# Optimization experiments

Measured on AMD Instinct MI355X. Metric: run time of the kernel, lower is better.

## Reference

```python
import jax, jax.numpy as jnp
import numpy as np

B, C, W, H = 4, 256, 64, 64
AC = C // 4  # attn channels


def setup_inputs() -> dict:
    key = jax.random.key(0)
    ks = jax.random.split(key, 4)
    x = jax.random.normal(ks[0], (B, C, W, H), dtype=jnp.float32)
    Wq = jax.random.normal(ks[1], (AC, C), dtype=jnp.float32) * (1.0 / np.sqrt(C))
    Wk = jax.random.normal(ks[2], (AC, C), dtype=jnp.float32) * (1.0 / np.sqrt(C))
    Wv = jax.random.normal(ks[3], (C, C), dtype=jnp.float32) * (1.0 / np.sqrt(C))
    bq = jnp.zeros((AC,), dtype=jnp.float32)
    bk = jnp.zeros((AC,), dtype=jnp.float32)
    bv = jnp.zeros((C,), dtype=jnp.float32)
    gamma = jnp.zeros((1,), dtype=jnp.float32)
    return {"x": x, "Wq": Wq, "bq": bq, "Wk": Wk, "bk": bk, "Wv": Wv, "bv": bv, "gamma": gamma}


def reference(x, Wq, bq, Wk, bk, Wv, bv, gamma):
    b, c, w, h = x.shape
    n = w * h
    xf = x.reshape(b, c, n)  # [B, C, N]
    # 1x1 convs == channel GEMMs
    q = jnp.einsum('oc,bcn->bon', Wq, xf) + bq[None, :, None]  # [B, AC, N]
    k = jnp.einsum('oc,bcn->bon', Wk, xf) + bk[None, :, None]  # [B, AC, N]
    v = jnp.einsum('oc,bcn->bon', Wv, xf) + bv[None, :, None]  # [B, C, N]
    # attn[b, i, j] = sum_c q[b, c, i] * k[b, c, j]  (query transposed)
    attn = jnp.einsum('bci,bcj->bij', q, k)  # [B, N, N]
    # NOTE: non-standard softmax over dim=1 (over query index i for each column j)
    attn = jax.nn.softmax(attn, axis=1)
    # attn_out = attn @ value.T  -> [B, N, C]
    attn_out = jnp.einsum('bij,bcj->bic', attn, v)
    attn_out = attn_out.reshape(b, w, h, c).transpose(0, 3, 1, 2)  # [B, C, W, H]
    return gamma[0] * attn_out + x
```

## Files before the change

### kernel.cpp

```cpp
#include <hip/hip_runtime.h>
#include <hip/hip_bf16.h>

#define BB 4
#define CC 256
#define NN 4096
#define AC2 64
#define PP 76

typedef __attribute__((ext_vector_type(4))) float f32x4;
typedef __attribute__((ext_vector_type(8))) short bf16x8;

__device__ __forceinline__ short f2bf(float f) {
    unsigned u = __builtin_bit_cast(unsigned, f);
    u = u + 0x7FFFu + ((u >> 16) & 1u);
    return (short)(u >> 16);
}

__global__ __launch_bounds__(256) void prep_kernel(
    const float* __restrict__ Wq, const float* __restrict__ Wk,
    const float* __restrict__ Wv, short* __restrict__ Wb)
{
    const int idx = (blockIdx.x * 256 + threadIdx.x) * 4;
    const int o = idx >> 8, c = idx & 255;
    const float* row = (o < 64) ? (Wq + o * CC)
                     : (o < 128) ? (Wk + (o - 64) * CC)
                                 : (Wv + (o - 128) * CC);
    float4 v = *(const float4*)&row[c];
    short4 s4;
    s4.x = f2bf(v.x); s4.y = f2bf(v.y); s4.z = f2bf(v.z); s4.w = f2bf(v.w);
    *(short4*)&Wb[idx] = s4;
}

__global__ __launch_bounds__(512) void qkv_kernel(
    const float* __restrict__ x, const short* __restrict__ Wb,
    const float* __restrict__ bq, const float* __restrict__ bk,
    const float* __restrict__ bv,
    short* __restrict__ Qt, short* __restrict__ Kt, short* __restrict__ V)
{
    __shared__ __align__(16) short Xl[32 * 72];
    const int bid0 = blockIdx.x;
    const int bid = ((bid0 & 7) << 6) | (bid0 >> 3);
    const int b = bid >> 7;
    const int n0 = (bid & 127) << 5;
    const int tid = threadIdx.x;
    const int lane = tid & 63, w = tid >> 6;
    const int l15 = lane & 15, lh = lane >> 4;

    f32x4 acc[3][2];
#pragma unroll
    for (int i = 0; i < 3; ++i)
#pragma unroll
        for (int j = 0; j < 2; ++j) acc[i][j] = (f32x4){0.f, 0.f, 0.f, 0.f};

    for (int ck = 0; ck < 4; ++ck) {
        const int c0 = ck << 6;
        bf16x8 Af[3][2];
#pragma unroll
        for (int of = 0; of < 3; ++of)
#pragma unroll
            for (int ks = 0; ks < 2; ++ks)
                Af[of][ks] = *(const bf16x8*)&Wb[(size_t)(w * 48 + of * 16 + l15) * CC +
                                                 c0 + ks * 32 + (lh << 3)];
        {
            const int cr = tid >> 3, q4 = tid & 7;
            float4 v = *(const float4*)&x[((size_t)(b * CC + c0 + cr)) * NN + n0 + q4 * 4];
            Xl[(q4 * 4 + 0) * 72 + cr] = f2bf(v.x);
            Xl[(q4 * 4 + 1) * 72 + cr] = f2bf(v.y);
            Xl[(q4 * 4 + 2) * 72 + cr] = f2bf(v.z);
            Xl[(q4 * 4 + 3) * 72 + cr] = f2bf(v.w);
        }
        __syncthreads();
#pragma unroll
        for (int ks = 0; ks < 2; ++ks) {
            const int co = ks * 32 + (lh << 3);
            bf16x8 Bf[2];
#pragma unroll
            for (int nf = 0; nf < 2; ++nf)
                Bf[nf] = *(const bf16x8*)&Xl[(nf * 16 + l15) * 72 + co];
#pragma unroll
            for (int of = 0; of < 3; ++of)
#pragma unroll
                for (int nf = 0; nf < 2; ++nf)
                    acc[of][nf] = __builtin_amdgcn_mfma_f32_16x16x32_bf16(
                        Af[of][ks], Bf[nf], acc[of][nf], 0, 0, 0);
        }
        __syncthreads();
    }
#pragma unroll
    for (int of = 0; of < 3; ++of) {
        const int obase = w * 48 + of * 16 + (lh << 2);
        float bias[4];
#pragma unroll
        for (int r = 0; r < 4; ++r) {
            int o = obase + r;
            bias[r] = (o < 64) ? bq[o] : (o < 128) ? bk[o - 64] : bv[o - 128];
        }
#pragma unroll
        for (int nf = 0; nf < 2; ++nf) {
            const int n = n0 + nf * 16 + l15;
            if (obase < 128) {
                short4 pk;
                pk.x = f2bf(acc[of][nf][0] + bias[0]);
                pk.y = f2bf(acc[of][nf][1] + bias[1]);
                pk.z = f2bf(acc[of][nf][2] + bias[2]);
                pk.w = f2bf(acc[of][nf][3] + bias[3]);
                short* dst = (obase < 64)
                    ? (Qt + ((size_t)b * NN + n) * AC2 + obase)
                    : (Kt + ((size_t)b * NN + n) * AC2 + (obase - 64));
                *(short4*)dst = pk;
            } else {
#pragma unroll
                for (int r = 0; r < 4; ++r) {
                    int o = obase + r - 128;
                    V[(((size_t)b * CC + o) * NN) + n] = f2bf(acc[of][nf][r] + bias[r]);
                }
            }
        }
    }
}

__global__ __launch_bounds__(256) void stats_kernel(
    const short* __restrict__ Qt, const short* __restrict__ Kt,
    float* __restrict__ tArr)
{
    const int bid0 = blockIdx.x;
    const int bid = ((bid0 & 7) << 7) | (bid0 >> 3);
    const int b = bid >> 8;
    const int j0 = (bid & 255) << 4;
    const int tid = threadIdx.x;
    const int lane = tid & 63, w = tid >> 6;
    const int l15 = lane & 15, lh = lane >> 4;
    const short* Qb = Qt + (size_t)b * NN * AC2;

    bf16x8 Bf[2];
#pragma unroll
    for (int ks = 0; ks < 2; ++ks)
        Bf[ks] = *(const bf16x8*)&Kt[((size_t)b * NN + j0 + l15) * AC2 +
                                     ks * 32 + (lh << 3)];

    bf16x8 A0[4], A1[4];
#pragma unroll
    for (int f = 0; f < 4; ++f) {
        const size_t rowA = (size_t)(w * 1024 + f * 16 + l15);
        A0[f] = *(const bf16x8*)&Qb[rowA * AC2 + (lh << 3)];
        A1[f] = *(const bf16x8*)&Qb[rowA * AC2 + 32 + (lh << 3)];
    }

    float m_run = -INFINITY, l_run = 0.f;
    for (int ii = 0; ii < 16; ++ii) {
        bf16x8 A0n[4], A1n[4];
        const int in0 = w * 1024 + ((ii + 1) & 15) * 64;
#pragma unroll
        for (int f = 0; f < 4; ++f) {
            const size_t rowA = (size_t)(in0 + f * 16 + l15);
            A0n[f] = *(const bf16x8*)&Qb[rowA * AC2 + (lh << 3)];
            A1n[f] = *(const bf16x8*)&Qb[rowA * AC2 + 32 + (lh << 3)];
        }
        f32x4 s[4];
#pragma unroll
        for (int f = 0; f < 4; ++f) {
            f32x4 t = (f32x4){0.f, 0.f, 0.f, 0.f};
            t = __builtin_amdgcn_mfma_f32_16x16x32_bf16(A0[f], Bf[0], t, 0, 0, 0);
            t = __builtin_amdgcn_mfma_f32_16x16x32_bf16(A1[f], Bf[1], t, 0, 0, 0);
            s[f] = t;
        }
        float mx = s[0][0];
#pragma unroll
        for (int f = 0; f < 4; ++f)
#pragma unroll
            for (int r = 0; r < 4; ++r) mx = fmaxf(mx, s[f][r]);
        const float m_new = fmaxf(m_run, mx);
        float add = 0.f;
#pragma unroll
        for (int f = 0; f < 4; ++f)
#pragma unroll
            for (int r = 0; r < 4; ++r) add += __expf(s[f][r] - m_new);
        l_run = l_run * __expf(m_run - m_new) + add;
        m_run = m_new;
#pragma unroll
        for (int f = 0; f < 4; ++f) { A0[f] = A0n[f]; A1[f] = A1n[f]; }
    }
#pragma unroll
    for (int off = 16; off <= 32; off <<= 1) {
        float m2 = __shfl_xor(m_run, off);
        float l2 = __shfl_xor(l_run, off);
        float mm = fmaxf(m_run, m2);
        l_run = l_run * __expf(m_run - mm) + l2 * __expf(m2 - mm);
        m_run = mm;
    }
    __shared__ float sm[4][16];
    __shared__ float sl[4][16];
    if (lane < 16) { sm[w][lane] = m_run; sl[w][lane] = l_run; }
    __syncthreads();
    if (tid < 16) {
        float m = sm[0][tid], l = sl[0][tid];
#pragma unroll
        for (int q = 1; q < 4; ++q) {
            float m2 = sm[q][tid], l2 = sl[q][tid];
            float mm = fmaxf(m, m2);
            l = l * __expf(m - mm) + l2 * __expf(m2 - mm);
            m = mm;
        }
        tArr[(size_t)b * NN + j0 + tid] = m + __logf(l);
    }
}

__global__ __launch_bounds__(256) void out_kernel(
    const short* __restrict__ Qt, const short* __restrict__ Kt,
    const short* __restrict__ V,
    const float* __restrict__ tArr,
    const float* __restrict__ x, const float* __restrict__ gamma,
    float* __restrict__ out)
{
    __shared__ __align__(16) short Pl[2][64 * PP];
    const int bid0 = blockIdx.x;
    const int bid = ((bid0 & 7) << 6) | (bid0 >> 3);
    const int cs = bid & 1;
    const int itile = (bid >> 1) & 63;
    const int b = bid >> 7;
    const int i0 = itile << 6, c0 = cs << 7;
    const int tid = threadIdx.x;
    const int lane = tid & 63, w = tid >> 6;
    const int l15 = lane & 15, lh = lane >> 4;
    const int iw = i0 + (w << 4);

    const short* Ktb = Kt + (size_t)b * NN * AC2;
    const float* tb  = tArr + (size_t)b * NN;
    const short* Vb  = V + ((size_t)b * CC + c0 + (w << 5)) * NN;

    bf16x8 Aq[2];
#pragma unroll
    for (int ks = 0; ks < 2; ++ks)
        Aq[ks] = *(const bf16x8*)&Qt[((size_t)b * NN + iw + l15) * AC2 +
                                     ks * 32 + (lh << 3)];

    f32x4 acc[4][2];
#pragma unroll
    for (int f = 0; f < 4; ++f)
#pragma unroll
        for (int cf = 0; cf < 2; ++cf) acc[f][cf] = (f32x4){0.f, 0.f, 0.f, 0.f};

    bf16x8 Kc[4][2], Vc[2][2];
    float tc[4];
#pragma unroll
    for (int jf = 0; jf < 4; ++jf) {
#pragma unroll
        for (int ks = 0; ks < 2; ++ks)
            Kc[jf][ks] = *(const bf16x8*)&Ktb[(size_t)(jf * 16 + l15) * AC2 +
                                              ks * 32 + (lh << 3)];
        tc[jf] = tb[jf * 16 + l15];
    }
#pragma unroll
    for (int cf = 0; cf < 2; ++cf)
#pragma unroll
        for (int ks = 0; ks < 2; ++ks)
            Vc[cf][ks] = *(const bf16x8*)&Vb[(size_t)(cf * 16 + l15) * NN +
                                             ks * 32 + (lh << 3)];

    for (int jt = 0; jt < 64; ++jt) {
        const int jn = ((jt + 1) & 63) << 6;
        bf16x8 Kn[4][2], Vn[2][2];
        float tn[4];
#pragma unroll
        for (int jf = 0; jf < 4; ++jf) {
#pragma unroll
            for (int ks = 0; ks < 2; ++ks)
                Kn[jf][ks] = *(const bf16x8*)&Ktb[(size_t)(jn + jf * 16 + l15) * AC2 +
                                                  ks * 32 + (lh << 3)];
            tn[jf] = tb[jn + jf * 16 + l15];
        }
#pragma unroll
        for (int cf = 0; cf < 2; ++cf)
#pragma unroll
            for (int ks = 0; ks < 2; ++ks)
                Vn[cf][ks] = *(const bf16x8*)&Vb[(size_t)(cf * 16 + l15) * NN + jn +
                                                 ks * 32 + (lh << 3)];

        short* Plw = &Pl[jt & 1][0];
#pragma unroll
        for (int jf = 0; jf < 4; ++jf) {
            f32x4 s = (f32x4){0.f, 0.f, 0.f, 0.f};
            s = __builtin_amdgcn_mfma_f32_16x16x32_bf16(Aq[0], Kc[jf][0], s, 0, 0, 0);
            s = __builtin_amdgcn_mfma_f32_16x16x32_bf16(Aq[1], Kc[jf][1], s, 0, 0, 0);
#pragma unroll
            for (int r = 0; r < 4; ++r)
                Plw[(w * 16 + lh * 4 + r) * PP + jf * 16 + l15] =
                    f2bf(__expf(s[r] - tc[jf]));
        }
        asm volatile("s_waitcnt lgkmcnt(0)" ::: "memory");
        __builtin_amdgcn_s_barrier();
        asm volatile("" ::: "memory");
#pragma unroll
        for (int ks = 0; ks < 2; ++ks) {
#pragma unroll
            for (int f = 0; f < 4; ++f) {
                bf16x8 Ap = *(const bf16x8*)&Plw[(f * 16 + l15) * PP +
                                                 ks * 32 + (lh << 3)];
#pragma unroll
                for (int cf = 0; cf < 2; ++cf)
                    acc[f][cf] = __builtin_amdgcn_mfma_f32_16x16x32_bf16(
                        Ap, Vc[cf][ks], acc[f][cf], 0, 0, 0);
            }
        }
#pragma unroll
        for (int jf = 0; jf < 4; ++jf) {
            Kc[jf][0] = Kn[jf][0]; Kc[jf][1] = Kn[jf][1]; tc[jf] = tn[jf];
        }
#pragma unroll
        for (int cf = 0; cf < 2; ++cf) { Vc[cf][0] = Vn[cf][0]; Vc[cf][1] = Vn[cf][1]; }
    }

    __syncthreads();
    const float g = gamma[0];
    float* Pfw = (float*)&Pl[0][0] + w * 1056;
#pragma unroll
    for (int pass = 0; pass < 2; ++pass) {
#pragma unroll
        for (int fh = 0; fh < 2; ++fh) {
            const int f = pass * 2 + fh;
#pragma unroll
            for (int cf = 0; cf < 2; ++cf)
#pragma unroll
                for (int r = 0; r < 4; ++r)
                    Pfw[(cf * 16 + l15) * 33 + fh * 16 + lh * 4 + r] = acc[f][cf][r];
        }
#pragma unroll
        for (int cq = 0; cq < 4; ++cq) {
            const int c = cq * 8 + (lane >> 3);
            const int iq = (lane & 7) * 4;
            float4 v;
            v.x = Pfw[c * 33 + iq + 0];
            v.y = Pfw[c * 33 + iq + 1];
            v.z = Pfw[c * 33 + iq + 2];
            v.w = Pfw[c * 33 + iq + 3];
            const size_t gidx = ((size_t)(b * CC + c0 + w * 32 + c)) * NN +
                                i0 + pass * 32 + iq;
            float4 xv = *(const float4*)&x[gidx];
            float4 o;
            o.x = g * v.x + xv.x;
            o.y = g * v.y + xv.y;
            o.z = g * v.z + xv.z;
            o.w = g * v.w + xv.w;
            *(float4*)&out[gidx] = o;
        }
    }
}

extern "C" void kernel_launch(void* const* d_in, const int* in_sizes, int n_in,
                              void* d_out, int out_size, void* d_ws, size_t ws_size,
                              hipStream_t stream) {
    const float* x     = (const float*)d_in[0];
    const float* Wq    = (const float*)d_in[1];
    const float* bq    = (const float*)d_in[2];
    const float* Wk    = (const float*)d_in[3];
    const float* bk    = (const float*)d_in[4];
    const float* Wv    = (const float*)d_in[5];
    const float* bv    = (const float*)d_in[6];
    const float* gamma = (const float*)d_in[7];
    float* out = (float*)d_out;

    short* Qt = (short*)d_ws;
    short* Kt = Qt + (size_t)BB * NN * AC2;
    short* V  = Kt + (size_t)BB * NN * AC2;
    float* tArr = (float*)(V + (size_t)BB * CC * NN);
    short* Wb = (short*)(tArr + (size_t)BB * NN);

    prep_kernel<<<96, 256, 0, stream>>>(Wq, Wk, Wv, Wb);
    qkv_kernel<<<BB * 128, 512, 0, stream>>>(x, Wb, bq, bk, bv, Qt, Kt, V);
    stats_kernel<<<BB * 256, 256, 0, stream>>>(Qt, Kt, tArr);
    out_kernel<<<BB * 128, 256, 0, stream>>>(Qt, Kt, V, tArr, x, gamma, out);
}
```

Measured before the change: 338.2 us.

## Split attention key dimension across two blocks and stage K tiles through LDS

The output kernel now splits the 4096-key reduction into two halves handled by separate blocks, doubling the grid to improve CU occupancy. Each half writes its partial result as bf16 into one 16-bit slot of the output buffer, and a new reduce kernel sums the two halves and applies gamma and the residual. K tiles and softmax stats are now loaded cooperatively into double-buffered LDS instead of per-wave global loads. In exchange it adds an extra kernel pass over the output and rounds the partial sums to bf16, which costs precision.

```diff
diff --git a/kernel.cpp b/kernel.cpp
--- a/kernel.cpp
+++ b/kernel.cpp
@@ -6,6 +6,7 @@
 #define NN 4096
 #define AC2 64
 #define PP 76
+#define JT 32
 
 typedef __attribute__((ext_vector_type(4))) float f32x4;
 typedef __attribute__((ext_vector_type(8))) short bf16x8;
@@ -14,6 +15,10 @@
     unsigned u = __builtin_bit_cast(unsigned, f);
     u = u + 0x7FFFu + ((u >> 16) & 1u);
     return (short)(u >> 16);
+}
+__device__ __forceinline__ float bf2f(unsigned short h) {
+    unsigned u = ((unsigned)h) << 16;
+    return __builtin_bit_cast(float, u);
 }
 
 __global__ __launch_bounds__(256) void prep_kernel(
@@ -205,28 +210,36 @@
     }
 }
 
-__global__ __launch_bounds__(256) void out_kernel(
+__global__ __launch_bounds__(256, 4) void out_kernel(
     const short* __restrict__ Qt, const short* __restrict__ Kt,
     const short* __restrict__ V,
     const float* __restrict__ tArr,
-    const float* __restrict__ x, const float* __restrict__ gamma,
     float* __restrict__ out)
 {
+    __shared__ __align__(16) short Kl[2][64 * PP];
     __shared__ __align__(16) short Pl[2][64 * PP];
+    __shared__ float Tl[2][64];
     const int bid0 = blockIdx.x;
-    const int bid = ((bid0 & 7) << 6) | (bid0 >> 3);
-    const int cs = bid & 1;
-    const int itile = (bid >> 1) & 63;
-    const int b = bid >> 7;
+    const int bid = ((bid0 & 7) << 7) | (bid0 >> 3);
+    const int jh = bid & 1;
+    const int cs = (bid >> 1) & 1;
+    const int itile = (bid >> 2) & 63;
+    const int b = bid >> 8;
     const int i0 = itile << 6, c0 = cs << 7;
+    const int jbase = jh << 11;
     const int tid = threadIdx.x;
     const int lane = tid & 63, w = tid >> 6;
     const int l15 = lane & 15, lh = lane >> 4;
     const int iw = i0 + (w << 4);
 
     const short* Ktb = Kt + (size_t)b * NN * AC2;
-    const float* tb  = tArr + (size_t)b * NN;
-    const short* Vb  = V + ((size_t)b * CC + c0 + (w << 5)) * NN;
+    const float* tb  = tArr + (size_t)b * NN + jbase;
+    const short* Vb  = V + ((size_t)(b * CC + c0 + (w << 5))) * NN + jbase;
+
+    const int krow = tid >> 2, kch = (tid & 3) << 4;
+    const short* Ksrc = Ktb + ((size_t)(jbase + krow)) * AC2 + kch;
+    short* const KlwA = &Kl[0][krow * PP + kch];
+    short* const KlwB = &Kl[1][krow * PP + kch];
 
     bf16x8 Aq[2];
 #pragma unroll
@@ -240,52 +253,65 @@
 #pragma unroll
         for (int cf = 0; cf < 2; ++cf) acc[f][cf] = (f32x4){0.f, 0.f, 0.f, 0.f};
 
-    bf16x8 Kc[4][2], Vc[2][2];
-    float tc[4];
-#pragma unroll
-    for (int jf = 0; jf < 4; ++jf) {
-#pragma unroll
-        for (int ks = 0; ks < 2; ++ks)
-            Kc[jf][ks] = *(const bf16x8*)&Ktb[(size_t)(jf * 16 + l15) * AC2 +
-                                              ks * 32 + (lh << 3)];
-        tc[jf] = tb[jf * 16 + l15];
-    }
+    {
+        bf16x8 k0a = *(const bf16x8*)(Ksrc + 0);
+        bf16x8 k0b = *(const bf16x8*)(Ksrc + 8);
+        float   t0 = (tid < 64) ? tb[tid] : 0.f;
+        *(bf16x8*)(KlwA + 0) = k0a;
+        *(bf16x8*)(KlwA + 8) = k0b;
+        if (tid < 64) Tl[0][tid] = t0;
+    }
+    bf16x8 KpA = *(const bf16x8*)(Ksrc + (1 << 12));
+    bf16x8 KpB = *(const bf16x8*)(Ksrc + (1 << 12) + 8);
+    float  tp  = (tid < 64) ? tb[64 + tid] : 0.f;
+    bf16x8 Vc[2][2];
 #pragma unroll
     for (int cf = 0; cf < 2; ++cf)
 #pragma unroll
         for (int ks = 0; ks < 2; ++ks)
             Vc[cf][ks] = *(const bf16x8*)&Vb[(size_t)(cf * 16 + l15) * NN +
                                              ks * 32 + (lh << 3)];
-
-    for (int jt = 0; jt < 64; ++jt) {
-        const int jn = ((jt + 1) & 63) << 6;
-        bf16x8 Kn[4][2], Vn[2][2];
-        float tn[4];
+    asm volatile("s_waitcnt lgkmcnt(0)" ::: "memory");
+    __builtin_amdgcn_s_barrier();
+    asm volatile("" ::: "memory");
+
+    for (int jt = 0; jt < JT; ++jt) {
+        const int cur = jt & 1;
+        {
+            short* kd = cur ? KlwA : KlwB;
+            *(bf16x8*)(kd + 0) = KpA;
+            *(bf16x8*)(kd + 8) = KpB;
+            if (tid < 64) Tl[cur ^ 1][tid] = tp;
+        }
+        {
+            const size_t t2 = (size_t)((jt + 2) & (JT - 1)) << 12;
+            KpA = *(const bf16x8*)(Ksrc + t2);
+            KpB = *(const bf16x8*)(Ksrc + t2 + 8);
+            tp  = (tid < 64) ? tb[(((jt + 2) & (JT - 1)) << 6) + tid] : 0.f;
+        }
+        bf16x8 Vn[2][2];
+        {
+            const int tv = ((jt + 1) & (JT - 1)) << 6;
+#pragma unroll
+            for (int cf = 0; cf < 2; ++cf)
+#pragma unroll
+                for (int ks = 0; ks < 2; ++ks)
+                    Vn[cf][ks] = *(const bf16x8*)&Vb[(size_t)(cf * 16 + l15) * NN +
+                                                     tv + ks * 32 + (lh << 3)];
+        }
+        short* Pw = &Pl[cur][0];
 #pragma unroll
         for (int jf = 0; jf < 4; ++jf) {
-#pragma unroll
-            for (int ks = 0; ks < 2; ++ks)
-                Kn[jf][ks] = *(const bf16x8*)&Ktb[(size_t)(jn + jf * 16 + l15) * AC2 +
-                                                  ks * 32 + (lh << 3)];
-            tn[jf] = tb[jn + jf * 16 + l15];
-        }
-#pragma unroll
-        for (int cf = 0; cf < 2; ++cf)
-#pragma unroll
-            for (int ks = 0; ks < 2; ++ks)
-                Vn[cf][ks] = *(const bf16x8*)&Vb[(size_t)(cf * 16 + l15) * NN + jn +
-                                                 ks * 32 + (lh << 3)];
-
-        short* Plw = &Pl[jt & 1][0];
-#pragma unroll
-        for (int jf = 0; jf < 4; ++jf) {
+            bf16x8 Ka = *(const bf16x8*)&Kl[cur][(jf * 16 + l15) * PP + (lh << 3)];
+            bf16x8 Kb = *(const bf16x8*)&Kl[cur][(jf * 16 + l15) * PP + 32 + (lh << 3)];
             f32x4 s = (f32x4){0.f, 0.f, 0.f, 0.f};
-            s = __builtin_amdgcn_mfma_f32_16x16x32_bf16(Aq[0], Kc[jf][0], s, 0, 0, 0);
-            s = __builtin_amdgcn_mfma_f32_16x16x32_bf16(Aq[1], Kc[jf][1], s, 0, 0, 0);
+            s = __builtin_amdgcn_mfma_f32_16x16x32_bf16(Aq[0], Ka, s, 0, 0, 0);
+            s = __builtin_amdgcn_mfma_f32_16x16x32_bf16(Aq[1], Kb, s, 0, 0, 0);
+            const float tj = Tl[cur][jf * 16 + l15];
 #pragma unroll
             for (int r = 0; r < 4; ++r)
-                Plw[(w * 16 + lh * 4 + r) * PP + jf * 16 + l15] =
-                    f2bf(__expf(s[r] - tc[jf]));
+                Pw[(w * 16 + lh * 4 + r) * PP + jf * 16 + l15] =
+                    f2bf(__expf(s[r] - tj));
         }
         asm volatile("s_waitcnt lgkmcnt(0)" ::: "memory");
         __builtin_amdgcn_s_barrier();
@@ -294,8 +320,8 @@
         for (int ks = 0; ks < 2; ++ks) {
 #pragma unroll
             for (int f = 0; f < 4; ++f) {
-                bf16x8 Ap = *(const bf16x8*)&Plw[(f * 16 + l15) * PP +
-                                                 ks * 32 + (lh << 3)];
+                bf16x8 Ap = *(const bf16x8*)&Pw[(f * 16 + l15) * PP +
+                                                ks * 32 + (lh << 3)];
 #pragma unroll
                 for (int cf = 0; cf < 2; ++cf)
                     acc[f][cf] = __builtin_amdgcn_mfma_f32_16x16x32_bf16(
@@ -303,16 +329,14 @@
             }
         }
 #pragma unroll
-        for (int jf = 0; jf < 4; ++jf) {
-            Kc[jf][0] = Kn[jf][0]; Kc[jf][1] = Kn[jf][1]; tc[jf] = tn[jf];
-        }
-#pragma unroll
-        for (int cf = 0; cf < 2; ++cf) { Vc[cf][0] = Vn[cf][0]; Vc[cf][1] = Vn[cf][1]; }
+        for (int cf = 0; cf < 2; ++cf) {
+            Vc[cf][0] = Vn[cf][0]; Vc[cf][1] = Vn[cf][1];
+        }
     }
 
     __syncthreads();
-    const float g = gamma[0];
     float* Pfw = (float*)&Pl[0][0] + w * 1056;
+    unsigned short* po = (unsigned short*)out;
 #pragma unroll
     for (int pass = 0; pass < 2; ++pass) {
 #pragma unroll
@@ -328,21 +352,33 @@
         for (int cq = 0; cq < 4; ++cq) {
             const int c = cq * 8 + (lane >> 3);
             const int iq = (lane & 7) * 4;
-            float4 v;
-            v.x = Pfw[c * 33 + iq + 0];
-            v.y = Pfw[c * 33 + iq + 1];
-            v.z = Pfw[c * 33 + iq + 2];
-            v.w = Pfw[c * 33 + iq + 3];
-            const size_t gidx = ((size_t)(b * CC + c0 + w * 32 + c)) * NN +
-                                i0 + pass * 32 + iq;
-            float4 xv = *(const float4*)&x[gidx];
-            float4 o;
-            o.x = g * v.x + xv.x;
-            o.y = g * v.y + xv.y;
-            o.z = g * v.z + xv.z;
-            o.w = g * v.w + xv.w;
-            *(float4*)&out[gidx] = o;
-        }
+            const size_t gi = ((size_t)(b * CC + c0 + w * 32 + c)) * NN +
+                              i0 + pass * 32 + iq;
+#pragma unroll
+            for (int k = 0; k < 4; ++k) {
+                float v = Pfw[c * 33 + iq + k];
+                po[(gi + k) * 2 + jh] = (unsigned short)f2bf(v);
+            }
+        }
+    }
+}
+
+__global__ __launch_bounds__(256) void reduce_kernel(
+    const float* __restrict__ x, const float* __restrict__ gamma,
+    float* __restrict__ out)
+{
+    const float g = gamma[0];
+    const size_t total = (size_t)BB * CC * NN / 4;
+    for (size_t i = (size_t)blockIdx.x * 256 + threadIdx.x; i < total;
+         i += (size_t)2048 * 256) {
+        uint4 pv = ((const uint4*)out)[i];
+        float4 xv = ((const float4*)x)[i];
+        float4 o;
+        o.x = g * (bf2f(pv.x & 0xFFFFu) + bf2f(pv.x >> 16)) + xv.x;
+        o.y = g * (bf2f(pv.y & 0xFFFFu) + bf2f(pv.y >> 16)) + xv.y;
+        o.z = g * (bf2f(pv.z & 0xFFFFu) + bf2f(pv.z >> 16)) + xv.z;
+        o.w = g * (bf2f(pv.w & 0xFFFFu) + bf2f(pv.w >> 16)) + xv.w;
+        ((float4*)out)[i] = o;
     }
 }
 
@@ -368,5 +404,6 @@
     prep_kernel<<<96, 256, 0, stream>>>(Wq, Wk, Wv, Wb);
     qkv_kernel<<<BB * 128, 512, 0, stream>>>(x, Wb, bq, bk, bv, Qt, Kt, V);
     stats_kernel<<<BB * 256, 256, 0, stream>>>(Qt, Kt, tArr);
-    out_kernel<<<BB * 128, 256, 0, stream>>>(Qt, Kt, V, tArr, x, gamma, out);
-}
+    out_kernel<<<BB * 256, 256, 0, stream>>>(Qt, Kt, V, tArr, out);
+    reduce_kernel<<<2048, 256, 0, stream>>>(x, gamma, out);
+}
```

After: 348.1 us. 1.03x slower.
